# Kernel optimization log

Measured on AMD Instinct MI355X. Metric: run time of the kernel, lower is better.

The kernel has to match this reference:

```python
import jax, jax.numpy as jnp
import numpy as np


def setup_inputs() -> dict:
    key = jax.random.key(0)
    k1, k2 = jax.random.split(key)
    B, S, D, R = 8, 2048, 1024, 128
    batch = jax.random.normal(k1, (B, S, D), dtype=jnp.float32)
    proj = jax.random.normal(k2, (D, R), dtype=jnp.float32) * (1.0 / np.sqrt(D))
    return {"batch": batch, "proj": proj}


def reference(batch, proj):
    # transformed: (B, S, R)
    t = jnp.matmul(batch, proj)
    # Pairwise squared L2 distances: ||ti||^2 + ||tj||^2 - 2 ti.tj
    # (same math as expand/diff/pow/sum, without the (B,S,S,R) intermediate)
    sq = jnp.sum(t * t, axis=-1)                       # (B, S)
    dots = jnp.einsum('bir,bjr->bij', t, t)            # (B, S, S)
    d2 = sq[:, :, None] + sq[:, None, :] - 2.0 * dots  # (B, S, S)
    return d2
```

## Files before the change

kernel.cpp:

```cpp
#include <hip/hip_runtime.h>
#include <hip/hip_bf16.h>

typedef short bf16x8 __attribute__((ext_vector_type(8)));
typedef float f32x4 __attribute__((ext_vector_type(4)));

#define NB 8
#define SS 2048
#define DD 1024
#define RR 128

__device__ __forceinline__ short f2bf(float x){
  unsigned u = __float_as_uint(x);
  u += 0x7fffu + ((u >> 16) & 1u);
  return (short)(u >> 16);
}
__device__ __forceinline__ float bf2f(short h){
  return __uint_as_float(((unsigned)(unsigned short)h) << 16);
}
__device__ __forceinline__ void gload16(const void* g, void* l){
  __builtin_amdgcn_global_load_lds((const __attribute__((address_space(1))) unsigned*)g,
                                   (__attribute__((address_space(3))) unsigned*)l, 16, 0, 0);
}
__device__ __forceinline__ int swz(int row, int c16){
  return row * 64 + ((c16 ^ (row & 7)) << 3);
}

__global__ __launch_bounds__(256) void k0_proj(const float* __restrict__ proj,
                                               short* __restrict__ pt_hi,
                                               short* __restrict__ pt_lo){
  __shared__ float tile[64][65];
  const int d0 = blockIdx.x * 64, r0 = blockIdx.y * 64;
  const int tid = threadIdx.x;
  #pragma unroll
  for (int i = 0; i < 16; ++i){
    int u = i * 256 + tid;
    int d = u >> 6, r = u & 63;
    tile[d][r] = proj[(d0 + d) * RR + r0 + r];
  }
  __syncthreads();
  #pragma unroll
  for (int i = 0; i < 16; ++i){
    int u = i * 256 + tid;
    int r = u >> 6, d = u & 63;
    float x = tile[d][r];
    short h = f2bf(x);
    short l = f2bf(x - bf2f(h));
    pt_hi[(r0 + r) * DD + d0 + d] = h;
    pt_lo[(r0 + r) * DD + d0 + d] = l;
  }
}

__global__ __launch_bounds__(512, 2) void k1_gemm1(const float* __restrict__ batch,
                                                   const short* __restrict__ pt_hi,
                                                   const short* __restrict__ pt_lo,
                                                   short* __restrict__ t_hi,
                                                   short* __restrict__ t_lo,
                                                   float* __restrict__ sqv){
  __shared__ short Ah[64 * 64], Al[64 * 64];
  __shared__ short Ph[128 * 64], Pl[128 * 64];
  __shared__ float sqpart[64];
  const int tid = threadIdx.x;
  const int w = tid >> 6, lane = tid & 63;
  const int lr = lane & 15, lg = lane >> 4;
  const int wr = w & 3, wc = w >> 2;
  const int row0 = blockIdx.x * 64;
  const int colg = (lane & 7) ^ (lane >> 3);
  if (tid < 64) sqpart[tid] = 0.f;
  f32x4 acc[4] = {{0.f,0.f,0.f,0.f}};
  #pragma unroll 1
  for (int k0 = 0; k0 < DD; k0 += 64){
    #pragma unroll
    for (int i = 0; i < 2; ++i){
      int u = tid * 2 + i;
      int r = u >> 4, kc = (u & 15) * 4;
      float4 v = *(const float4*)(batch + (size_t)(row0 + r) * DD + k0 + kc);
      short4 hv, lv;
      hv.x = f2bf(v.x); lv.x = f2bf(v.x - bf2f(hv.x));
      hv.y = f2bf(v.y); lv.y = f2bf(v.y - bf2f(hv.y));
      hv.z = f2bf(v.z); lv.z = f2bf(v.z - bf2f(hv.z));
      hv.w = f2bf(v.w); lv.w = f2bf(v.w - bf2f(hv.w));
      int sidx = r * 64 + (((kc >> 3) ^ (r & 7)) << 3) + (kc & 7);
      *(short4*)&Ah[sidx] = hv;
      *(short4*)&Al[sidx] = lv;
    }
    #pragma unroll
    for (int q = 0; q < 2; ++q){
      int prow = w * 16 + q * 8 + (lane >> 3);
      const short* gh = pt_hi + prow * DD + k0 + colg * 8;
      const short* gl = pt_lo + prow * DD + k0 + colg * 8;
      gload16(gh, &Ph[w * 1024 + q * 512]);
      gload16(gl, &Pl[w * 1024 + q * 512]);
    }
    __syncthreads();
    #pragma unroll
    for (int ks = 0; ks < 2; ++ks){
      int c16 = ks * 4 + lg;
      bf16x8 ah = *(const bf16x8*)&Ah[swz(wr * 16 + lr, c16)];
      bf16x8 al = *(const bf16x8*)&Al[swz(wr * 16 + lr, c16)];
      bf16x8 bh[4], bl[4];
      #pragma unroll
      for (int n = 0; n < 4; ++n){
        int prow = wc * 64 + n * 16 + lr;
        bh[n] = *(const bf16x8*)&Ph[swz(prow, c16)];
        bl[n] = *(const bf16x8*)&Pl[swz(prow, c16)];
      }
      #pragma unroll
      for (int n = 0; n < 4; ++n)
        acc[n] = __builtin_amdgcn_mfma_f32_16x16x32_bf16(ah, bh[n], acc[n], 0, 0, 0);
      #pragma unroll
      for (int n = 0; n < 4; ++n)
        acc[n] = __builtin_amdgcn_mfma_f32_16x16x32_bf16(ah, bl[n], acc[n], 0, 0, 0);
      #pragma unroll
      for (int n = 0; n < 4; ++n)
        acc[n] = __builtin_amdgcn_mfma_f32_16x16x32_bf16(al, bh[n], acc[n], 0, 0, 0);
    }
    __syncthreads();
  }
  #pragma unroll
  for (int r = 0; r < 4; ++r){
    int lrow = wr * 16 + lg * 4 + r;
    int grow = row0 + lrow;
    float s = 0.f;
    #pragma unroll
    for (int n = 0; n < 4; ++n){
      float x = acc[n][r];
      s += x * x;
      int col = wc * 64 + n * 16 + lr;
      short h = f2bf(x);
      short l = f2bf(x - bf2f(h));
      t_hi[(size_t)grow * RR + col] = h;
      t_lo[(size_t)grow * RR + col] = l;
    }
    s += __shfl_xor(s, 1);
    s += __shfl_xor(s, 2);
    s += __shfl_xor(s, 4);
    s += __shfl_xor(s, 8);
    if (lr == 0) atomicAdd(&sqpart[lrow], s);
  }
  __syncthreads();
  if (tid < 64) sqv[row0 + tid] = sqpart[tid];
}

__global__ __launch_bounds__(256, 2) void k2_dist(const short* __restrict__ t_hi,
                                                  const short* __restrict__ t_lo,
                                                  const float* __restrict__ sqv,
                                                  float* __restrict__ out){
  __shared__ short Ah[128 * 64], Al[128 * 64];
  __shared__ short Bh[128 * 64], Bl[128 * 64];
  const int tid = threadIdx.x;
  const int w = tid >> 6, lane = tid & 63;
  const int lr = lane & 15, lg = lane >> 4;
  const int bi = blockIdx.z;
  int p = blockIdx.x;
  int ti = 0;
  while (p >= 16 - ti){ p -= 16 - ti; ++ti; }
  const int tj = ti + p;
  const int i0 = ti * 128, j0 = tj * 128;
  const size_t tbase = (size_t)bi * SS * RR;
  const int colg = (lane & 7) ^ (lane >> 3);

  f32x4 acc[16] = {{0.f,0.f,0.f,0.f}};
  #pragma unroll 1
  for (int k0 = 0; k0 < RR; k0 += 64){
    #pragma unroll
    for (int q = 0; q < 4; ++q){
      int rloc = w * 32 + q * 8 + (lane >> 3);
      size_t goffA = tbase + (size_t)(i0 + rloc) * RR + k0 + colg * 8;
      size_t goffB = tbase + (size_t)(j0 + rloc) * RR + k0 + colg * 8;
      int ldst = w * 2048 + q * 512;
      gload16(t_hi + goffA, &Ah[ldst]);
      gload16(t_lo + goffA, &Al[ldst]);
      gload16(t_hi + goffB, &Bh[ldst]);
      gload16(t_lo + goffB, &Bl[ldst]);
    }
    __syncthreads();
    #pragma unroll
    for (int ks = 0; ks < 2; ++ks){
      int c16 = ks * 4 + lg;
      bf16x8 ah[2], al[2];
      #pragma unroll
      for (int rt = 0; rt < 2; ++rt){
        int arow = w * 32 + rt * 16 + lr;
        ah[rt] = *(const bf16x8*)&Ah[swz(arow, c16)];
        al[rt] = *(const bf16x8*)&Al[swz(arow, c16)];
      }
      bf16x8 bh[8], bl[8];
      #pragma unroll
      for (int n = 0; n < 8; ++n){
        int brow = n * 16 + lr;
        bh[n] = *(const bf16x8*)&Bh[swz(brow, c16)];
        bl[n] = *(const bf16x8*)&Bl[swz(brow, c16)];
      }
      #pragma unroll
      for (int rt = 0; rt < 2; ++rt)
        #pragma unroll
        for (int n = 0; n < 8; ++n)
          acc[rt * 8 + n] = __builtin_amdgcn_mfma_f32_16x16x32_bf16(ah[rt], bh[n], acc[rt * 8 + n], 0, 0, 0);
      #pragma unroll
      for (int rt = 0; rt < 2; ++rt)
        #pragma unroll
        for (int n = 0; n < 8; ++n)
          acc[rt * 8 + n] = __builtin_amdgcn_mfma_f32_16x16x32_bf16(ah[rt], bl[n], acc[rt * 8 + n], 0, 0, 0);
      #pragma unroll
      for (int rt = 0; rt < 2; ++rt)
        #pragma unroll
        for (int n = 0; n < 8; ++n)
          acc[rt * 8 + n] = __builtin_amdgcn_mfma_f32_16x16x32_bf16(al[rt], bh[n], acc[rt * 8 + n], 0, 0, 0);
    }
    __syncthreads();
  }
  float* outb = out + (size_t)bi * SS * SS;
  const float* sqb = sqv + bi * SS;
  float sqj_reg[8];
  #pragma unroll
  for (int n = 0; n < 8; ++n) sqj_reg[n] = sqb[j0 + n * 16 + lr];
  #pragma unroll
  for (int rt = 0; rt < 2; ++rt){
    int rbase = w * 32 + rt * 16 + lg * 4;
    float sqi_reg[4];
    #pragma unroll
    for (int r = 0; r < 4; ++r) sqi_reg[r] = sqb[i0 + rbase + r];
    #pragma unroll
    for (int n = 0; n < 8; ++n){
      int col = n * 16 + lr;
      float4 mv;
      #pragma unroll
      for (int r = 0; r < 4; ++r){
        int row = rbase + r;
        float v = sqi_reg[r] + sqj_reg[n] - 2.0f * acc[rt * 8 + n][r];
        outb[(size_t)(i0 + row) * SS + (j0 + col)] = v;
        ((float*)&mv)[r] = v;
      }
      if (ti != tj)
        *(float4*)&outb[(size_t)(j0 + col) * SS + (i0 + rbase)] = mv;
    }
  }
}

extern "C" void kernel_launch(void* const* d_in, const int* in_sizes, int n_in,
                              void* d_out, int out_size, void* d_ws, size_t ws_size,
                              hipStream_t stream) {
  const float* batch = (const float*)d_in[0];
  const float* proj  = (const float*)d_in[1];
  float* out = (float*)d_out;
  char* ws = (char*)d_ws;

  short* pt_hi = (short*)(ws);
  short* pt_lo = (short*)(ws + 262144);
  short* t_hi  = (short*)(ws + 524288);
  short* t_lo  = (short*)(ws + 4718592);
  float* sqv   = (float*)(ws + 8912896);

  k0_proj<<<dim3(16, 2), 256, 0, stream>>>(proj, pt_hi, pt_lo);
  k1_gemm1<<<dim3(256), 512, 0, stream>>>(batch, pt_hi, pt_lo, t_hi, t_lo, sqv);
  k2_dist<<<dim3(136, 1, 8), 256, 0, stream>>>(t_hi, t_lo, sqv, out);
}
```

Before: 224.9 us.

## Stage GEMM outputs through LDS for coalesced vectorized global stores

k1 now writes the bf16 hi/lo split of t into shared memory (reusing the P buffers) and then copies it to global memory with 16-byte coalesced stores, replacing scattered 2-byte stores. k2 stages the accumulator tile in LDS so the direct (non-transposed) output block is written as row-contiguous float4 stores instead of scalar stores, while the mirrored block keeps its float4 stores taken from registers. The grid is reordered so the batch index varies fastest, which changes which blocks are resident together. This adds a barrier and LDS traffic per block, and the 64KB ftile reuse of the operand buffers may limit occupancy.

```diff
diff --git a/kernel.cpp b/kernel.cpp
--- a/kernel.cpp
+++ b/kernel.cpp
@@ -56,9 +56,12 @@
                                                    short* __restrict__ t_hi,
                                                    short* __restrict__ t_lo,
                                                    float* __restrict__ sqv){
-  __shared__ short Ah[64 * 64], Al[64 * 64];
-  __shared__ short Ph[128 * 64], Pl[128 * 64];
-  __shared__ float sqpart[64];
+  __shared__ __align__(16) char smem[49408];
+  short* Ah = (short*)smem;
+  short* Al = (short*)(smem + 8192);
+  short* Ph = (short*)(smem + 16384);
+  short* Pl = (short*)(smem + 32768);
+  float* sqpart = (float*)(smem + 49152);
   const int tid = threadIdx.x;
   const int w = tid >> 6, lane = tid & 63;
   const int lr = lane & 15, lg = lane >> 4;
@@ -116,10 +119,11 @@
     }
     __syncthreads();
   }
+  short* Th = Ph;
+  short* Tl = Pl;
   #pragma unroll
   for (int r = 0; r < 4; ++r){
     int lrow = wr * 16 + lg * 4 + r;
-    int grow = row0 + lrow;
     float s = 0.f;
     #pragma unroll
     for (int n = 0; n < 4; ++n){
@@ -128,8 +132,8 @@
       int col = wc * 64 + n * 16 + lr;
       short h = f2bf(x);
       short l = f2bf(x - bf2f(h));
-      t_hi[(size_t)grow * RR + col] = h;
-      t_lo[(size_t)grow * RR + col] = l;
+      Th[lrow * 128 + col] = h;
+      Tl[lrow * 128 + col] = l;
     }
     s += __shfl_xor(s, 1);
     s += __shfl_xor(s, 2);
@@ -138,6 +142,13 @@
     if (lr == 0) atomicAdd(&sqpart[lrow], s);
   }
   __syncthreads();
+  #pragma unroll
+  for (int ps = 0; ps < 2; ++ps){
+    int u = ps * 512 + tid;
+    int row = u >> 4, c8 = (u & 15) * 8;
+    *(int4*)&t_hi[(size_t)(row0 + row) * RR + c8] = *(int4*)&Th[row * 128 + c8];
+    *(int4*)&t_lo[(size_t)(row0 + row) * RR + c8] = *(int4*)&Tl[row * 128 + c8];
+  }
   if (tid < 64) sqv[row0 + tid] = sqpart[tid];
 }
 
@@ -145,13 +156,17 @@
                                                   const short* __restrict__ t_lo,
                                                   const float* __restrict__ sqv,
                                                   float* __restrict__ out){
-  __shared__ short Ah[128 * 64], Al[128 * 64];
-  __shared__ short Bh[128 * 64], Bl[128 * 64];
+  __shared__ __align__(16) char smem[65536];
+  short* Ah = (short*)smem;
+  short* Al = (short*)(smem + 16384);
+  short* Bh = (short*)(smem + 32768);
+  short* Bl = (short*)(smem + 49152);
+  float* ftile = (float*)smem;
   const int tid = threadIdx.x;
   const int w = tid >> 6, lane = tid & 63;
   const int lr = lane & 15, lg = lane >> 4;
-  const int bi = blockIdx.z;
-  int p = blockIdx.x;
+  const int bi = blockIdx.x;
+  int p = blockIdx.y;
   int ti = 0;
   while (p >= 16 - ti){ p -= 16 - ti; ++ti; }
   const int tj = ti + p;
@@ -211,28 +226,44 @@
   }
   float* outb = out + (size_t)bi * SS * SS;
   const float* sqb = sqv + bi * SS;
-  float sqj_reg[8];
-  #pragma unroll
-  for (int n = 0; n < 8; ++n) sqj_reg[n] = sqb[j0 + n * 16 + lr];
-  #pragma unroll
-  for (int rt = 0; rt < 2; ++rt){
-    int rbase = w * 32 + rt * 16 + lg * 4;
-    float sqi_reg[4];
-    #pragma unroll
-    for (int r = 0; r < 4; ++r) sqi_reg[r] = sqb[i0 + rbase + r];
-    #pragma unroll
-    for (int n = 0; n < 8; ++n){
-      int col = n * 16 + lr;
-      float4 mv;
-      #pragma unroll
-      for (int r = 0; r < 4; ++r){
-        int row = rbase + r;
-        float v = sqi_reg[r] + sqj_reg[n] - 2.0f * acc[rt * 8 + n][r];
-        outb[(size_t)(i0 + row) * SS + (j0 + col)] = v;
-        ((float*)&mv)[r] = v;
-      }
-      if (ti != tj)
-        *(float4*)&outb[(size_t)(j0 + col) * SS + (i0 + rbase)] = mv;
+  #pragma unroll
+  for (int rt = 0; rt < 2; ++rt)
+    #pragma unroll
+    for (int n = 0; n < 8; ++n)
+      #pragma unroll
+      for (int r = 0; r < 4; ++r)
+        ftile[(w * 32 + rt * 16 + lg * 4 + r) * 128 + n * 16 + lr] = acc[rt * 8 + n][r];
+  __syncthreads();
+  #pragma unroll
+  for (int v = 0; v < 16; ++v){
+    int u = v * 256 + tid;
+    int row = u >> 5, c4 = (u & 31) * 4;
+    float4 d = *(float4*)&ftile[row * 128 + c4];
+    float si = sqb[i0 + row];
+    float4 sj = *(const float4*)&sqb[j0 + c4];
+    float4 o;
+    o.x = si + sj.x - 2.0f * d.x;
+    o.y = si + sj.y - 2.0f * d.y;
+    o.z = si + sj.z - 2.0f * d.z;
+    o.w = si + sj.w - 2.0f * d.w;
+    *(float4*)&outb[(size_t)(i0 + row) * SS + j0 + c4] = o;
+  }
+  if (ti != tj){
+    #pragma unroll
+    for (int rt = 0; rt < 2; ++rt){
+      int rbase = w * 32 + rt * 16 + lg * 4;
+      float4 si4 = *(const float4*)&sqb[i0 + rbase];
+      #pragma unroll
+      for (int n = 0; n < 8; ++n){
+        int col = n * 16 + lr;
+        float sj = sqb[j0 + col];
+        float4 mv;
+        mv.x = si4.x + sj - 2.0f * acc[rt * 8 + n][0];
+        mv.y = si4.y + sj - 2.0f * acc[rt * 8 + n][1];
+        mv.z = si4.z + sj - 2.0f * acc[rt * 8 + n][2];
+        mv.w = si4.w + sj - 2.0f * acc[rt * 8 + n][3];
+        *(float4*)&outb[(size_t)(j0 + col) * SS + i0 + rbase] = mv;
+      }
     }
   }
 }
@@ -253,5 +284,5 @@
 
   k0_proj<<<dim3(16, 2), 256, 0, stream>>>(proj, pt_hi, pt_lo);
   k1_gemm1<<<dim3(256), 512, 0, stream>>>(batch, pt_hi, pt_lo, t_hi, t_lo, sqv);
-  k2_dist<<<dim3(136, 1, 8), 256, 0, stream>>>(t_hi, t_lo, sqv, out);
-}
+  k2_dist<<<dim3(8, 136), 256, 0, stream>>>(t_hi, t_lo, sqv, out);
+}
```

Measured after the change: 215.3 us. 1.04x faster.
